# Kernel tuning notes

Hardware: AMD Instinct MI355X
Metric: run time of the kernel (lower is better)

Reference implementation:

```python
import jax, jax.numpy as jnp
import numpy as np

EPSILON = 1e-8

def setup_inputs() -> dict:
    key = jax.random.key(0)
    k1, k2, k3, k4 = jax.random.split(key, 4)
    B, C_in, C_out, H, W, S, K = 16, 512, 512, 32, 32, 512, 3
    x = jax.random.normal(k1, (B, C_in, H, W), dtype=jnp.float32)
    w = jax.random.normal(k2, (B, S), dtype=jnp.float32)
    # Linear(style_dim -> in_chan), bias initialized to ones per module code
    style_w = jax.random.normal(k3, (C_in, S), dtype=jnp.float32) * (1.0 / np.sqrt(S))
    style_b = jnp.ones((C_in,), dtype=jnp.float32)
    # kaiming_normal_(fan_in, leaky_relu): std = sqrt(2/(1+0.01^2)) / sqrt(fan_in)
    fan_in = C_in * K * K
    gain = np.sqrt(2.0 / (1.0 + 0.01 ** 2))
    weight = jax.random.normal(k4, (C_out, C_in, K, K), dtype=jnp.float32) * (gain / np.sqrt(fan_in))
    return {"x": x, "w": w, "style_w": style_w, "style_b": style_b, "weight": weight}

def reference(x, w, style_w, style_b, weight):
    B, C, H, W_ = x.shape
    C_out, _, K, _ = weight.shape
    # style modulation: Linear(style_dim -> in_chan)
    style = w @ style_w.T + style_b                       # (B, C_in)
    weights = style[:, None, :, None, None] * weight[None]  # (B, C_out, C_in, K, K)
    # demodulation
    d = jax.lax.rsqrt(jnp.sum(weights * weights, axis=(2, 3, 4), keepdims=True) + EPSILON)
    weights = weights * d
    # grouped conv with groups = batch
    pad = 1 if K > 1 else 0
    xg = x.reshape(1, B * C, H, W_)
    wg = weights.reshape(B * C_out, C, K, K)
    y = jax.lax.conv_general_dilated(
        xg, wg, window_strides=(1, 1), padding=((pad, pad), (pad, pad)),
        dimension_numbers=("NCHW", "OIHW", "NCHW"), feature_group_count=B)
    return y.reshape(B, C_out, H, W_)
```

## Files before the change

kernel.cpp:

```cpp
#include <hip/hip_runtime.h>
#include <hip/hip_bf16.h>

#define NB 16
#define CI 512
#define CO 512
#define HW 1024
#define SD 512
#define EPSI 1e-8f

typedef __attribute__((ext_vector_type(8))) short bf16x8;
typedef __attribute__((ext_vector_type(16))) float f32x16;
typedef __attribute__((ext_vector_type(4))) unsigned int u32x4;

#define GLOAD_LDS16(g, l) __builtin_amdgcn_global_load_lds( \
    (const __attribute__((address_space(1))) unsigned int*)(const void*)(g), \
    (__attribute__((address_space(3))) unsigned int*)(void*)(l), 16, 0, 0)
#define SCHED0() __builtin_amdgcn_sched_barrier(0)
#define SBAR()   __builtin_amdgcn_s_barrier()

__global__ void k_style2(const float* __restrict__ w, const float* __restrict__ sw,
                         const float* __restrict__ sb, float* __restrict__ style) {
    int gw = (blockIdx.x * 256 + threadIdx.x) >> 6;
    int l = threadIdx.x & 63;
    int b = gw >> 9, c = gw & 511;
    const float4* wr = (const float4*)(w + b * SD) + (l << 1);
    const float4* sr = (const float4*)(sw + c * SD) + (l << 1);
    float4 a0 = wr[0], a1 = wr[1], q0 = sr[0], q1 = sr[1];
    float acc = a0.x * q0.x + a0.y * q0.y + a0.z * q0.z + a0.w * q0.w
              + a1.x * q1.x + a1.y * q1.y + a1.z * q1.z + a1.w * q1.w;
#pragma unroll
    for (int off = 32; off > 0; off >>= 1) acc += __shfl_down(acc, off);
    if (l == 0) style[gw] = acc + sb[c];
}

__global__ void k_wprep(const float* __restrict__ wt, float* __restrict__ wsq,
                        __hip_bfloat16* __restrict__ wtb, u32x4* __restrict__ zpage) {
    if (blockIdx.x == 0 && threadIdx.x < 64)
        zpage[threadIdx.x] = (u32x4){0, 0, 0, 0};
    int idx = blockIdx.x * 256 + threadIdx.x;
    const float* p = wt + idx * 9;
    float a = 0.f;
#pragma unroll
    for (int t = 0; t < 9; ++t) {
        float v = p[t];
        a += v * v;
        wtb[t * (CO * CI) + idx] = __float2bfloat16(v);
    }
    wsq[idx] = a;
}

__global__ void k_demod2(const float* __restrict__ style, const float* __restrict__ wsq,
                         float* __restrict__ dv) {
    int gw = (blockIdx.x * 256 + threadIdx.x) >> 6;
    int l = threadIdx.x & 63;
    int b = gw >> 9, co = gw & 511;
    const float4* st = (const float4*)(style + b * CI) + (l << 1);
    const float4* wq = (const float4*)(wsq + co * CI) + (l << 1);
    float4 s0 = st[0], s1 = st[1], q0 = wq[0], q1 = wq[1];
    float acc = s0.x * s0.x * q0.x + s0.y * s0.y * q0.y + s0.z * s0.z * q0.z + s0.w * s0.w * q0.w
              + s1.x * s1.x * q1.x + s1.y * s1.y * q1.y + s1.z * s1.z * q1.z + s1.w * s1.w * q1.w;
#pragma unroll
    for (int off = 32; off > 0; off >>= 1) acc += __shfl_down(acc, off);
    if (l == 0) dv[gw] = rsqrtf(acc + EPSI);
}

__global__ void k_xs(const float* __restrict__ x, const float* __restrict__ style,
                     __hip_bfloat16* __restrict__ xs) {
    __shared__ float tile[32][33];
    int b = blockIdx.z, c0 = blockIdx.y * 32, p0 = blockIdx.x * 32;
    int tx = threadIdx.x & 31, ty = threadIdx.x >> 5;
#pragma unroll
    for (int i = 0; i < 4; ++i) {
        int ci = c0 + ty + i * 8;
        tile[ty + i * 8][tx] = x[(b * CI + ci) * HW + p0 + tx] * style[b * CI + ci];
    }
    __syncthreads();
#pragma unroll
    for (int i = 0; i < 4; ++i) {
        int p = p0 + ty + i * 8;
        xs[(b * HW + p) * CI + c0 + tx] = __float2bfloat16(tile[tx][ty + i * 8]);
    }
}

#define XS_BYTES 52224
#define WBUF_BYTES 16384
#define SMEM_TOTAL (2 * XS_BYTES + 3 * WBUF_BYTES)

extern "C" __global__ __launch_bounds__(512, 2) void k_conv(
        const __hip_bfloat16* __restrict__ wtb,
        const __hip_bfloat16* __restrict__ xs,
        const float* __restrict__ dvec,
        const char* __restrict__ zpage,
        float* __restrict__ out) {
    extern __shared__ char smem[];
    char* Xs  = smem;
    char* Wsb = smem + 2 * XS_BYTES;

    const int tid  = threadIdx.x;
    const int lane = tid & 63;
    const int wv   = tid >> 6;
    const int wb   = wv >> 2;
    const int wr   = (wv >> 1) & 1;
    const int wn   = wv & 1;

    int bid = blockIdx.x;
    int xcd = bid & 7, idx = bid >> 3;
    int cot = xcd >> 1;
    int px8 = idx & 7;
    int bp  = (idx >> 3) | ((xcd & 1) << 2);
    const int co0 = cot * 128;
    const int p0  = px8 * 128;
    const int y0  = px8 * 4;
    const int b0  = bp * 2;
    const int b   = b0 + wb;

    if (tid < 192) {
        int g = tid & 7;
        int rx = ((tid >> 3) & 1) ? 33 : 0;
        int row = tid >> 4;
        int off = (row * 34 + rx) * 128 + g * 16;
        *(u32x4*)(Xs + off) = (u32x4){0, 0, 0, 0};
        *(u32x4*)(Xs + XS_BYTES + off) = (u32x4){0, 0, 0, 0};
    }

    const int srcgW = (lane & 7) ^ (lane >> 3);

    auto issueW = [&](int tap, int cin, int bufi) {
        const __hip_bfloat16* wsrc = wtb + ((size_t)tap * CO + co0) * CI + cin;
        char* wdst = Wsb + bufi * WBUF_BYTES;
#pragma unroll
        for (int k = 0; k < 2; ++k) {
            int seg = k * 8 + wv;
            int co_l = seg * 8 + (lane >> 3);
            GLOAD_LDS16(wsrc + co_l * CI + srcgW * 8, wdst + seg * 1024);
        }
    };
    auto issueX = [&](char* Xdst, int cin) {
#pragma unroll
        for (int k = 0; k < 6; ++k) {
            int sid = k * 8 + wv;
            int bb = (sid >= 24) ? 1 : 0;
            int rem = sid - bb * 24;
            int ry = rem >> 2, seg = rem & 3;
            int rx0 = 1 + seg * 8;
            char* ldst = Xdst + ((bb * 6 + ry) * 34 + rx0) * 128;
            int y = y0 - 1 + ry;
            int rx = rx0 + (lane >> 3);
            int srcg = (lane & 7) ^ (rx & 7);
            if ((unsigned)y < 32u)
                GLOAD_LDS16(xs + ((size_t)(b0 + bb) * HW + (y << 5) + (rx - 1)) * CI + cin + srcg * 8, ldst);
            else
                GLOAD_LDS16(zpage, ldst);
        }
    };

    f32x16 acc[2][2];
#pragma unroll
    for (int m = 0; m < 2; ++m)
#pragma unroll
        for (int n = 0; n < 2; ++n)
            acc[m][n] = (f32x16)(0.f);

    issueW(0, 0, 0);
    issueW(1, 0, 1);
    issueX(Xs, 0);
    SCHED0();
    asm volatile("s_waitcnt lgkmcnt(0) vmcnt(0)" ::: "memory");
    SCHED0();
    SBAR();
    SCHED0();

    for (int cc = 0; cc < 8; ++cc) {
        const char* Xcur = Xs + (cc & 1) * XS_BYTES;
#pragma unroll
        for (int t = 0; t < 9; ++t) {
            if (!(cc == 7 && t >= 7)) {
                const int tn  = (t <= 6) ? (t + 2) : (t - 7);
                const int cin = ((t <= 6) ? cc : (cc + 1)) * 64;
                issueW(tn, cin, (t + 2) % 3);
            }
            if (t == 0 && cc < 7)
                issueX(Xs + ((cc + 1) & 1) * XS_BYTES, (cc + 1) * 64);
            SCHED0();

            const char* Wb = Wsb + (t % 3) * WBUF_BYTES;
            const int ky = t / 3, kx = t - (t / 3) * 3;
            __builtin_amdgcn_s_setprio(1);
#pragma unroll
            for (int q = 0; q < 4; ++q) {
                bf16x8 afr[2], bfr[2];
                int g = (q << 1) + (lane >> 5);
#pragma unroll
                for (int m = 0; m < 2; ++m) {
                    int cr = wr * 64 + m * 32 + (lane & 31);
                    afr[m] = *(const bf16x8*)(Wb + cr * 128 + ((g ^ (cr & 7)) << 4));
                }
#pragma unroll
                for (int n = 0; n < 2; ++n) {
                    int ry = wn * 2 + n + ky;
                    int rx = (lane & 31) + kx;
                    bfr[n] = *(const bf16x8*)(Xcur + ((wb * 6 + ry) * 34 + rx) * 128 +
                                              ((g ^ (rx & 7)) << 4));
                }
#pragma unroll
                for (int m = 0; m < 2; ++m)
#pragma unroll
                    for (int n = 0; n < 2; ++n)
                        acc[m][n] = __builtin_amdgcn_mfma_f32_32x32x16_bf16(afr[m], bfr[n], acc[m][n], 0, 0, 0);
            }
            __builtin_amdgcn_s_setprio(0);

            if (!(cc == 7 && t == 8)) {
                SCHED0();
                if (cc < 7 && t < 2)
                    asm volatile("s_waitcnt lgkmcnt(0) vmcnt(8)" ::: "memory");
                else if (cc == 7 && t == 7)
                    asm volatile("s_waitcnt lgkmcnt(0) vmcnt(0)" ::: "memory");
                else
                    asm volatile("s_waitcnt lgkmcnt(0) vmcnt(2)" ::: "memory");
                SCHED0();
                SBAR();
                SCHED0();
            }
        }
    }

#pragma unroll
    for (int m = 0; m < 2; ++m) {
#pragma unroll
        for (int r = 0; r < 16; ++r) {
            int co = co0 + wr * 64 + m * 32 + (r & 3) + ((r >> 2) << 3) + ((lane >> 5) << 2);
            float dvv = dvec[b * CO + co];
            float* orow = out + ((size_t)b * CO + co) * HW + p0 + wn * 64;
            orow[lane & 31]        = acc[m][0][r] * dvv;
            orow[32 + (lane & 31)] = acc[m][1][r] * dvv;
        }
    }
}

extern "C" void kernel_launch(void* const* d_in, const int* in_sizes, int n_in,
                              void* d_out, int out_size, void* d_ws, size_t ws_size,
                              hipStream_t stream) {
    const float* x  = (const float*)d_in[0];
    const float* w  = (const float*)d_in[1];
    const float* sw = (const float*)d_in[2];
    const float* sb = (const float*)d_in[3];
    const float* wt = (const float*)d_in[4];
    float* out = (float*)d_out;

    char* ws = (char*)d_ws;
    float* style = (float*)(ws);
    float* dvec  = (float*)(ws + 32768);
    float* wsq   = (float*)(ws + 65536);
    __hip_bfloat16* wtb = (__hip_bfloat16*)(ws + 1114112);
    __hip_bfloat16* xsb = (__hip_bfloat16*)(ws + 5832704);
    char* zpage = ws + 22609920;

    hipFuncSetAttribute((const void*)k_conv,
                        hipFuncAttributeMaxDynamicSharedMemorySize, SMEM_TOTAL);

    k_style2<<<2048, 256, 0, stream>>>(w, sw, sb, style);
    k_wprep<<<1024, 256, 0, stream>>>(wt, wsq, (__hip_bfloat16*)wtb, (u32x4*)zpage);
    k_xs<<<dim3(32, 16, 16), 256, 0, stream>>>(x, style, xsb);
    k_demod2<<<2048, 256, 0, stream>>>(style, wsq, dvec);
    k_conv<<<256, 512, SMEM_TOTAL, stream>>>(wtb, xsb, dvec, zpage, out);
}
```

Measured before the change: 95.00 us.

## Split conv blocks to one batch per 256-thread block, single-buffer X tile

The conv kernel now uses 512 blocks of 256 threads, each handling one batch element instead of two. The X tile is single-buffered, so LDS per block is roughly halved and more blocks can be resident per CU. The next channel chunk's X load is now issued after the last tap, behind a barrier and a full wait, rather than prefetched during compute. This exposes a global-load stall once per channel chunk in exchange for higher occupancy, and each block reloads the weight tiles without sharing them across two batches.

```diff
diff --git a/kernel.cpp b/kernel.cpp
--- a/kernel.cpp
+++ b/kernel.cpp
@@ -82,11 +82,11 @@
     }
 }
 
-#define XS_BYTES 52224
+#define XS_BYTES 26112
 #define WBUF_BYTES 16384
-#define SMEM_TOTAL (2 * XS_BYTES + 3 * WBUF_BYTES)
-
-extern "C" __global__ __launch_bounds__(512, 2) void k_conv(
+#define SMEM_TOTAL (XS_BYTES + 3 * WBUF_BYTES)
+
+extern "C" __global__ __launch_bounds__(256, 2) void k_conv(
         const __hip_bfloat16* __restrict__ wtb,
         const __hip_bfloat16* __restrict__ xs,
         const float* __restrict__ dvec,
@@ -94,33 +94,28 @@
         float* __restrict__ out) {
     extern __shared__ char smem[];
     char* Xs  = smem;
-    char* Wsb = smem + 2 * XS_BYTES;
+    char* Wsb = smem + XS_BYTES;
 
     const int tid  = threadIdx.x;
     const int lane = tid & 63;
     const int wv   = tid >> 6;
-    const int wb   = wv >> 2;
-    const int wr   = (wv >> 1) & 1;
+    const int wr   = wv >> 1;
     const int wn   = wv & 1;
 
     int bid = blockIdx.x;
     int xcd = bid & 7, idx = bid >> 3;
-    int cot = xcd >> 1;
-    int px8 = idx & 7;
-    int bp  = (idx >> 3) | ((xcd & 1) << 2);
+    const int cot = xcd >> 1;
+    const int px8 = idx & 7;
+    const int b   = (idx >> 3) | ((xcd & 1) << 3);
     const int co0 = cot * 128;
     const int p0  = px8 * 128;
     const int y0  = px8 * 4;
-    const int b0  = bp * 2;
-    const int b   = b0 + wb;
-
-    if (tid < 192) {
+
+    if (tid < 96) {
         int g = tid & 7;
-        int rx = ((tid >> 3) & 1) ? 33 : 0;
+        int rx = (tid & 8) ? 33 : 0;
         int row = tid >> 4;
-        int off = (row * 34 + rx) * 128 + g * 16;
-        *(u32x4*)(Xs + off) = (u32x4){0, 0, 0, 0};
-        *(u32x4*)(Xs + XS_BYTES + off) = (u32x4){0, 0, 0, 0};
+        *(u32x4*)(Xs + (row * 34 + rx) * 128 + g * 16) = (u32x4){0, 0, 0, 0};
     }
 
     const int srcgW = (lane & 7) ^ (lane >> 3);
@@ -129,26 +124,24 @@
         const __hip_bfloat16* wsrc = wtb + ((size_t)tap * CO + co0) * CI + cin;
         char* wdst = Wsb + bufi * WBUF_BYTES;
 #pragma unroll
-        for (int k = 0; k < 2; ++k) {
-            int seg = k * 8 + wv;
+        for (int k = 0; k < 4; ++k) {
+            int seg = k * 4 + wv;
             int co_l = seg * 8 + (lane >> 3);
             GLOAD_LDS16(wsrc + co_l * CI + srcgW * 8, wdst + seg * 1024);
         }
     };
-    auto issueX = [&](char* Xdst, int cin) {
+    auto issueX = [&](int cin) {
 #pragma unroll
         for (int k = 0; k < 6; ++k) {
-            int sid = k * 8 + wv;
-            int bb = (sid >= 24) ? 1 : 0;
-            int rem = sid - bb * 24;
-            int ry = rem >> 2, seg = rem & 3;
+            int sid = k * 4 + wv;
+            int ry = sid >> 2, seg = sid & 3;
             int rx0 = 1 + seg * 8;
-            char* ldst = Xdst + ((bb * 6 + ry) * 34 + rx0) * 128;
+            char* ldst = Xs + (ry * 34 + rx0) * 128;
             int y = y0 - 1 + ry;
             int rx = rx0 + (lane >> 3);
             int srcg = (lane & 7) ^ (rx & 7);
             if ((unsigned)y < 32u)
-                GLOAD_LDS16(xs + ((size_t)(b0 + bb) * HW + (y << 5) + (rx - 1)) * CI + cin + srcg * 8, ldst);
+                GLOAD_LDS16(xs + ((size_t)b * HW + (y << 5) + (rx - 1)) * CI + cin + srcg * 8, ldst);
             else
                 GLOAD_LDS16(zpage, ldst);
         }
@@ -163,7 +156,7 @@
 
     issueW(0, 0, 0);
     issueW(1, 0, 1);
-    issueX(Xs, 0);
+    issueX(0);
     SCHED0();
     asm volatile("s_waitcnt lgkmcnt(0) vmcnt(0)" ::: "memory");
     SCHED0();
@@ -171,7 +164,6 @@
     SCHED0();
 
     for (int cc = 0; cc < 8; ++cc) {
-        const char* Xcur = Xs + (cc & 1) * XS_BYTES;
 #pragma unroll
         for (int t = 0; t < 9; ++t) {
             if (!(cc == 7 && t >= 7)) {
@@ -179,8 +171,6 @@
                 const int cin = ((t <= 6) ? cc : (cc + 1)) * 64;
                 issueW(tn, cin, (t + 2) % 3);
             }
-            if (t == 0 && cc < 7)
-                issueX(Xs + ((cc + 1) & 1) * XS_BYTES, (cc + 1) * 64);
             SCHED0();
 
             const char* Wb = Wsb + (t % 3) * WBUF_BYTES;
@@ -199,7 +189,7 @@
                 for (int n = 0; n < 2; ++n) {
                     int ry = wn * 2 + n + ky;
                     int rx = (lane & 31) + kx;
-                    bfr[n] = *(const bf16x8*)(Xcur + ((wb * 6 + ry) * 34 + rx) * 128 +
+                    bfr[n] = *(const bf16x8*)(Xs + ((ry * 34 + rx) * 128) +
                                               ((g ^ (rx & 7)) << 4));
                 }
 #pragma unroll
@@ -210,14 +200,28 @@
             }
             __builtin_amdgcn_s_setprio(0);
 
-            if (!(cc == 7 && t == 8)) {
-                SCHED0();
-                if (cc < 7 && t < 2)
-                    asm volatile("s_waitcnt lgkmcnt(0) vmcnt(8)" ::: "memory");
-                else if (cc == 7 && t == 7)
-                    asm volatile("s_waitcnt lgkmcnt(0) vmcnt(0)" ::: "memory");
-                else
-                    asm volatile("s_waitcnt lgkmcnt(0) vmcnt(2)" ::: "memory");
+            if (cc == 7 && t == 8) {
+            } else if (t == 8) {
+                SCHED0();
+                asm volatile("s_waitcnt lgkmcnt(0)" ::: "memory");
+                SCHED0();
+                SBAR();
+                SCHED0();
+                issueX((cc + 1) * 64);
+                SCHED0();
+                asm volatile("s_waitcnt lgkmcnt(0) vmcnt(0)" ::: "memory");
+                SCHED0();
+                SBAR();
+                SCHED0();
+            } else if (cc == 7 && t == 7) {
+                SCHED0();
+                asm volatile("s_waitcnt lgkmcnt(0) vmcnt(0)" ::: "memory");
+                SCHED0();
+                SBAR();
+                SCHED0();
+            } else {
+                SCHED0();
+                asm volatile("s_waitcnt lgkmcnt(0) vmcnt(4)" ::: "memory");
                 SCHED0();
                 SBAR();
                 SCHED0();
@@ -263,5 +267,5 @@
     k_wprep<<<1024, 256, 0, stream>>>(wt, wsq, (__hip_bfloat16*)wtb, (u32x4*)zpage);
     k_xs<<<dim3(32, 16, 16), 256, 0, stream>>>(x, style, xsb);
     k_demod2<<<2048, 256, 0, stream>>>(style, wsq, dvec);
-    k_conv<<<256, 512, SMEM_TOTAL, stream>>>(wtb, xsb, dvec, zpage, out);
-}
+    k_conv<<<512, 256, SMEM_TOTAL, stream>>>(wtb, xsb, dvec, zpage, out);
+}
```

Result: slower. 99.90 us (+5.2%).

## Merge prep kernels, fold demodulation into conv, vectorize xs transpose stores

Applied to the files above, without the earlier changes.

Merges the style and weight-prep kernels into one launch. Removes the separate demodulation kernel: each conv block now computes the demod factors it needs into LDS while the first tile loads are in flight. Also widens the xs transpose tile to 64 channels so each thread writes 16-byte bf16 vectors. This cuts launch overhead and uncoalesced stores, at the cost of redundant demod work per block and slightly more LDS use.

```diff
diff --git a/kernel.cpp b/kernel.cpp
--- a/kernel.cpp
+++ b/kernel.cpp
@@ -18,83 +18,73 @@
 #define SCHED0() __builtin_amdgcn_sched_barrier(0)
 #define SBAR()   __builtin_amdgcn_s_barrier()
 
-__global__ void k_style2(const float* __restrict__ w, const float* __restrict__ sw,
-                         const float* __restrict__ sb, float* __restrict__ style) {
-    int gw = (blockIdx.x * 256 + threadIdx.x) >> 6;
-    int l = threadIdx.x & 63;
-    int b = gw >> 9, c = gw & 511;
-    const float4* wr = (const float4*)(w + b * SD) + (l << 1);
-    const float4* sr = (const float4*)(sw + c * SD) + (l << 1);
-    float4 a0 = wr[0], a1 = wr[1], q0 = sr[0], q1 = sr[1];
-    float acc = a0.x * q0.x + a0.y * q0.y + a0.z * q0.z + a0.w * q0.w
-              + a1.x * q1.x + a1.y * q1.y + a1.z * q1.z + a1.w * q1.w;
-#pragma unroll
-    for (int off = 32; off > 0; off >>= 1) acc += __shfl_down(acc, off);
-    if (l == 0) style[gw] = acc + sb[c];
-}
-
-__global__ void k_wprep(const float* __restrict__ wt, float* __restrict__ wsq,
-                        __hip_bfloat16* __restrict__ wtb, u32x4* __restrict__ zpage) {
-    if (blockIdx.x == 0 && threadIdx.x < 64)
-        zpage[threadIdx.x] = (u32x4){0, 0, 0, 0};
-    int idx = blockIdx.x * 256 + threadIdx.x;
-    const float* p = wt + idx * 9;
-    float a = 0.f;
-#pragma unroll
-    for (int t = 0; t < 9; ++t) {
-        float v = p[t];
-        a += v * v;
-        wtb[t * (CO * CI) + idx] = __float2bfloat16(v);
-    }
-    wsq[idx] = a;
-}
-
-__global__ void k_demod2(const float* __restrict__ style, const float* __restrict__ wsq,
-                         float* __restrict__ dv) {
-    int gw = (blockIdx.x * 256 + threadIdx.x) >> 6;
-    int l = threadIdx.x & 63;
-    int b = gw >> 9, co = gw & 511;
-    const float4* st = (const float4*)(style + b * CI) + (l << 1);
-    const float4* wq = (const float4*)(wsq + co * CI) + (l << 1);
-    float4 s0 = st[0], s1 = st[1], q0 = wq[0], q1 = wq[1];
-    float acc = s0.x * s0.x * q0.x + s0.y * s0.y * q0.y + s0.z * s0.z * q0.z + s0.w * s0.w * q0.w
-              + s1.x * s1.x * q1.x + s1.y * s1.y * q1.y + s1.z * s1.z * q1.z + s1.w * s1.w * q1.w;
-#pragma unroll
-    for (int off = 32; off > 0; off >>= 1) acc += __shfl_down(acc, off);
-    if (l == 0) dv[gw] = rsqrtf(acc + EPSI);
+__global__ void k_prep(const float* __restrict__ w, const float* __restrict__ sw,
+                       const float* __restrict__ sb, const float* __restrict__ wt,
+                       float* __restrict__ style, float* __restrict__ wsq,
+                       __hip_bfloat16* __restrict__ wtb, u32x4* __restrict__ zpage) {
+    if (blockIdx.x < 2048) {
+        int gw = (blockIdx.x * 256 + threadIdx.x) >> 6;
+        int l = threadIdx.x & 63;
+        int b = gw >> 9, c = gw & 511;
+        const float4* wr = (const float4*)(w + b * SD) + (l << 1);
+        const float4* sr = (const float4*)(sw + c * SD) + (l << 1);
+        float4 a0 = wr[0], a1 = wr[1], q0 = sr[0], q1 = sr[1];
+        float acc = a0.x * q0.x + a0.y * q0.y + a0.z * q0.z + a0.w * q0.w
+                  + a1.x * q1.x + a1.y * q1.y + a1.z * q1.z + a1.w * q1.w;
+#pragma unroll
+        for (int off = 32; off > 0; off >>= 1) acc += __shfl_down(acc, off);
+        if (l == 0) style[gw] = acc + sb[c];
+    } else {
+        if (blockIdx.x == 2048 && threadIdx.x < 64)
+            zpage[threadIdx.x] = (u32x4){0, 0, 0, 0};
+        int idx = (blockIdx.x - 2048) * 256 + threadIdx.x;
+        const float* p = wt + idx * 9;
+        float a = 0.f;
+#pragma unroll
+        for (int t = 0; t < 9; ++t) {
+            float v = p[t];
+            a += v * v;
+            wtb[t * (CO * CI) + idx] = __float2bfloat16(v);
+        }
+        wsq[idx] = a;
+    }
 }
 
 __global__ void k_xs(const float* __restrict__ x, const float* __restrict__ style,
                      __hip_bfloat16* __restrict__ xs) {
-    __shared__ float tile[32][33];
-    int b = blockIdx.z, c0 = blockIdx.y * 32, p0 = blockIdx.x * 32;
+    __shared__ float tile[32][66];
+    int b = blockIdx.z, c0 = blockIdx.y * 64, p0 = blockIdx.x * 32;
     int tx = threadIdx.x & 31, ty = threadIdx.x >> 5;
 #pragma unroll
-    for (int i = 0; i < 4; ++i) {
-        int ci = c0 + ty + i * 8;
-        tile[ty + i * 8][tx] = x[(b * CI + ci) * HW + p0 + tx] * style[b * CI + ci];
+    for (int i = 0; i < 8; ++i) {
+        int ci = i * 8 + ty;
+        tile[tx][ci] = x[((size_t)b * CI + c0 + ci) * HW + p0 + tx] * style[b * CI + c0 + ci];
     }
     __syncthreads();
-#pragma unroll
-    for (int i = 0; i < 4; ++i) {
-        int p = p0 + ty + i * 8;
-        xs[(b * HW + p) * CI + c0 + tx] = __float2bfloat16(tile[tx][ty + i * 8]);
-    }
+    int r = threadIdx.x >> 3, kc = threadIdx.x & 7;
+    union { bf16x8 v; __hip_bfloat16 h[8]; } U;
+#pragma unroll
+    for (int i = 0; i < 8; ++i)
+        U.h[i] = __float2bfloat16(tile[r][kc * 8 + i]);
+    *(bf16x8*)(xs + ((size_t)b * HW + p0 + r) * CI + c0 + kc * 8) = U.v;
 }
 
 #define XS_BYTES 52224
 #define WBUF_BYTES 16384
-#define SMEM_TOTAL (2 * XS_BYTES + 3 * WBUF_BYTES)
+#define DV_OFF (2 * XS_BYTES + 3 * WBUF_BYTES)
+#define SMEM_TOTAL (DV_OFF + 1024)
 
 extern "C" __global__ __launch_bounds__(512, 2) void k_conv(
         const __hip_bfloat16* __restrict__ wtb,
         const __hip_bfloat16* __restrict__ xs,
-        const float* __restrict__ dvec,
+        const float* __restrict__ style,
+        const float* __restrict__ wsq,
         const char* __restrict__ zpage,
         float* __restrict__ out) {
     extern __shared__ char smem[];
     char* Xs  = smem;
     char* Wsb = smem + 2 * XS_BYTES;
+    float* dvLDS = (float*)(smem + DV_OFF);
 
     const int tid  = threadIdx.x;
     const int lane = tid & 63;
@@ -164,6 +154,20 @@
     issueW(0, 0, 0);
     issueW(1, 0, 1);
     issueX(Xs, 0);
+    {
+        int idx2 = tid >> 1, h = tid & 1;
+        int bb = idx2 >> 7, col = idx2 & 127;
+        const float4* wq = (const float4*)(wsq + (size_t)(co0 + col) * CI) + h * 64;
+        const float4* st = (const float4*)(style + (size_t)(b0 + bb) * CI) + h * 64;
+        float a = 0.f;
+#pragma unroll 4
+        for (int i = 0; i < 64; ++i) {
+            float4 q = wq[i], s = st[i];
+            a += s.x * s.x * q.x + s.y * s.y * q.y + s.z * s.z * q.z + s.w * s.w * q.w;
+        }
+        a += __shfl_down(a, 1);
+        if (!h) dvLDS[idx2] = rsqrtf(a + EPSI);
+    }
     SCHED0();
     asm volatile("s_waitcnt lgkmcnt(0) vmcnt(0)" ::: "memory");
     SCHED0();
@@ -229,9 +233,9 @@
     for (int m = 0; m < 2; ++m) {
 #pragma unroll
         for (int r = 0; r < 16; ++r) {
-            int co = co0 + wr * 64 + m * 32 + (r & 3) + ((r >> 2) << 3) + ((lane >> 5) << 2);
-            float dvv = dvec[b * CO + co];
-            float* orow = out + ((size_t)b * CO + co) * HW + p0 + wn * 64;
+            int col = wr * 64 + m * 32 + (r & 3) + ((r >> 2) << 3) + ((lane >> 5) << 2);
+            float dvv = dvLDS[wb * 128 + col];
+            float* orow = out + ((size_t)b * CO + co0 + col) * HW + p0 + wn * 64;
             orow[lane & 31]        = acc[m][0][r] * dvv;
             orow[32 + (lane & 31)] = acc[m][1][r] * dvv;
         }
@@ -250,7 +254,6 @@
 
     char* ws = (char*)d_ws;
     float* style = (float*)(ws);
-    float* dvec  = (float*)(ws + 32768);
     float* wsq   = (float*)(ws + 65536);
     __hip_bfloat16* wtb = (__hip_bfloat16*)(ws + 1114112);
     __hip_bfloat16* xsb = (__hip_bfloat16*)(ws + 5832704);
@@ -259,9 +262,8 @@
     hipFuncSetAttribute((const void*)k_conv,
                         hipFuncAttributeMaxDynamicSharedMemorySize, SMEM_TOTAL);
 
-    k_style2<<<2048, 256, 0, stream>>>(w, sw, sb, style);
-    k_wprep<<<1024, 256, 0, stream>>>(wt, wsq, (__hip_bfloat16*)wtb, (u32x4*)zpage);
-    k_xs<<<dim3(32, 16, 16), 256, 0, stream>>>(x, style, xsb);
-    k_demod2<<<2048, 256, 0, stream>>>(style, wsq, dvec);
-    k_conv<<<256, 512, SMEM_TOTAL, stream>>>(wtb, xsb, dvec, zpage, out);
-}
+    k_prep<<<3072, 256, 0, stream>>>(w, sw, sb, wt, style, wsq,
+                                     (__hip_bfloat16*)wtb, (u32x4*)zpage);
+    k_xs<<<dim3(32, 8, 16), 256, 0, stream>>>(x, style, xsb);
+    k_conv<<<256, 512, SMEM_TOTAL, stream>>>(wtb, xsb, style, wsq, zpage, out);
+}
```

New measurement: 109.0 us (median of 2 runs). 14.8% more time.
